# Kernel tuning notes

Hardware: AMD Instinct MI355X
Metric: run time of the kernel (lower is better)

Reference implementation:

```python
import jax, jax.numpy as jnp
import numpy as np

N_HEAD = 16
R = 4  # reciprocal rank

def setup_inputs() -> dict:
    key = jax.random.key(0)
    ks = jax.random.split(key, 8)
    B, T, C = 2, 2048, 1024
    H = N_HEAD
    D = C // H
    D_std = D - R
    x = jax.random.normal(ks[0], (B, T, C), dtype=jnp.float32)
    W_attn = jax.random.normal(ks[1], (3 * C, C), dtype=jnp.float32) * (1.0 / np.sqrt(C))
    W_proj = jax.random.normal(ks[2], (C, C), dtype=jnp.float32) * (1.0 / np.sqrt(C))
    w_std = jnp.full((H,), D_std / D, dtype=jnp.float32)
    w_rec = jnp.full((H,), R / D, dtype=jnp.float32)
    skip_std = jnp.float32(2.0)
    skip_low = jnp.float32(-3.0)
    rwr_alpha = jnp.full((H,), 0.05, dtype=jnp.float32)
    return {"x": x, "W_attn": W_attn, "W_proj": W_proj, "w_std": w_std,
            "w_rec": w_rec, "skip_std": skip_std, "skip_low": skip_low,
            "rwr_alpha": rwr_alpha}

def reference(x, W_attn, W_proj, w_std, w_rec, skip_std, skip_low, rwr_alpha):
    B, T, C = x.shape
    H = N_HEAD
    D = C // H
    D_std = D - R
    # fused QKV projection: [Qf | Kf | V]
    fused = jnp.einsum('btc,fc->btf', x, W_attn)
    qf, kf, v = jnp.split(fused, 3, axis=-1)
    Qf = qf.reshape(B, T, H, D).transpose(0, 2, 1, 3)  # (B,H,T,D)
    Kf = kf.reshape(B, T, H, D).transpose(0, 2, 1, 3)
    V = v.reshape(B, T, H, D).transpose(0, 2, 1, 3)
    # dynamic per-head gate scaling folded into Qf/Kf
    g_std = jnp.sqrt(jnp.clip(w_std * jax.nn.sigmoid(skip_std), 1e-8))  # (H,)
    g_rec = jnp.sqrt(jnp.clip(w_rec * jax.nn.sigmoid(skip_low), 1e-8))  # (H,)
    scale = jnp.concatenate([
        jnp.broadcast_to(g_std[:, None], (H, D_std)),
        jnp.broadcast_to(g_rec[:, None], (H, R)),
    ], axis=-1)  # (H, D)
    scale = scale[None, :, None, :]  # (1,H,1,D)
    Qf = Qf * scale
    Kf = Kf * scale
    # causal SDPA (scale = 1/sqrt(head_dim), dropout=0)
    scores = jnp.einsum('bhqd,bhkd->bhqk', Qf, Kf) / jnp.sqrt(jnp.float32(D))
    causal = jnp.tril(jnp.ones((T, T), dtype=bool))
    scores = jnp.where(causal[None, None], scores, jnp.float32(-1e30))
    attn = jax.nn.softmax(scores, axis=-1)
    y = jnp.einsum('bhqk,bhkd->bhqd', attn, V)
    # self-restart mix: out = (1-alpha)*attn_out + alpha*V, alpha in [0, 0.5]
    alpha = jnp.clip(rwr_alpha, 0.0, 0.5)[None, :, None, None]
    y = (1.0 - alpha) * y + alpha * V
    y = y.transpose(0, 2, 1, 3).reshape(B, T, C)
    return jnp.einsum('btc,oc->bto', y, W_proj)
```

## Files before the change

kernel.cpp:

```cpp
#include <hip/hip_runtime.h>
#include <hip/hip_bf16.h>
#include <math.h>
#include <stdint.h>

#define B_    2
#define T_    2048
#define C_    1024
#define H_    16
#define D_    64
#define R_    4
#define DSTD  60
#define F_    3072
#define BT_   (B_ * T_)

#define LOG2E 1.44269504088896340736f

typedef __bf16 bf16x8 __attribute__((ext_vector_type(8)));
typedef __bf16 bf16x4 __attribute__((ext_vector_type(4)));
typedef float  f32x4  __attribute__((ext_vector_type(4)));

__device__ __forceinline__ int swz(int row, int blk) {
    return blk ^ ((row >> 1) & 7);
}

__device__ __forceinline__ void st_pair(__bf16* p, __bf16 a, __bf16 b) {
    union { __bf16 h[2]; uint32_t u; } t;
    t.h[0] = a; t.h[1] = b;
    *(uint32_t*)p = t.u;
}

__device__ __forceinline__ void gload_lds16(const void* g, void* l) {
    __builtin_amdgcn_global_load_lds(
        (const __attribute__((address_space(1))) uint32_t*)g,
        (__attribute__((address_space(3))) uint32_t*)l, 16, 0, 0);
}

__global__ __launch_bounds__(256) void cast3_kernel(
    const float* __restrict__ a, int na4,
    const float* __restrict__ b, int nb4,
    const float* __restrict__ c, int nc4,
    __bf16* __restrict__ oa, __bf16* __restrict__ ob, __bf16* __restrict__ oc)
{
    int i = blockIdx.x * 256 + threadIdx.x;
    const float* s; __bf16* d; int j = i;
    if (j < na4) { s = a; d = oa; }
    else {
        j -= na4;
        if (j < nb4) { s = b; d = ob; }
        else {
            j -= nb4;
            if (j >= nc4) return;
            s = c; d = oc;
        }
    }
    float4 v = ((const float4*)s)[j];
    bf16x4 o;
    o[0] = (__bf16)v.x; o[1] = (__bf16)v.y;
    o[2] = (__bf16)v.z; o[3] = (__bf16)v.w;
    ((bf16x4*)d)[j] = o;
}

__global__ __launch_bounds__(256) void gemm_qkv_kernel(
    const __bf16* __restrict__ A,
    const __bf16* __restrict__ Bw,
    const float* __restrict__ w_std, const float* __restrict__ w_rec,
    const float* __restrict__ skip_std, const float* __restrict__ skip_low,
    __bf16* __restrict__ Q, __bf16* __restrict__ K, __bf16* __restrict__ V)
{
    __shared__ __bf16 As[128 * 32];
    __shared__ __bf16 Bs[128 * 32];

    const int tid  = threadIdx.x;
    const int row0 = blockIdx.x * 128;
    const int col0 = blockIdx.y * 128;

    const int w    = tid >> 6;
    const int lane = tid & 63;
    const int quad = lane >> 4;
    const int lt   = lane & 15;
    const int wm   = w >> 1;
    const int wn   = w & 1;

    const int lrow = tid >> 2;
    const int lcol = (tid & 3) * 8;

    f32x4 acc[4][4];
#pragma unroll
    for (int i = 0; i < 4; ++i)
#pragma unroll
        for (int j = 0; j < 4; ++j)
#pragma unroll
            for (int r = 0; r < 4; ++r) acc[i][j][r] = 0.f;

    for (int kt = 0; kt < C_ / 32; ++kt) {
        const int k0 = kt * 32;
        __syncthreads();
#pragma unroll
        for (int rr = 0; rr < 2; ++rr) {
            gload_lds16(A  + (size_t)(row0 + rr * 64 + lrow) * C_ + k0 + lcol,
                        As + rr * 2048 + tid * 8);
            gload_lds16(Bw + (size_t)(col0 + rr * 64 + lrow) * C_ + k0 + lcol,
                        Bs + rr * 2048 + tid * 8);
        }
        __syncthreads();

        bf16x8 af[4], bf[4];
#pragma unroll
        for (int i = 0; i < 4; ++i)
            af[i] = *(const bf16x8*)&As[(wm * 64 + i * 16 + lt) * 32 + quad * 8];
#pragma unroll
        for (int j = 0; j < 4; ++j)
            bf[j] = *(const bf16x8*)&Bs[(wn * 64 + j * 16 + lt) * 32 + quad * 8];
#pragma unroll
        for (int i = 0; i < 4; ++i)
#pragma unroll
            for (int j = 0; j < 4; ++j)
                acc[i][j] = __builtin_amdgcn_mfma_f32_16x16x32_bf16(af[i], bf[j], acc[i][j], 0, 0, 0);
    }

    const int colbase = col0 + wn * 64;
    const int which   = colbase >> 10;
    const int h       = (colbase & (C_ - 1)) >> 6;

    const float ss = 1.f / (1.f + __expf(-skip_std[0]));
    const float sl = 1.f / (1.f + __expf(-skip_low[0]));
    const float gs = sqrtf(fmaxf(w_std[h] * ss, 1e-8f));
    const float gr = sqrtf(fmaxf(w_rec[h] * sl, 1e-8f));

    __bf16* dstM = (which == 0) ? Q : (which == 1) ? K : V;

#pragma unroll
    for (int i = 0; i < 4; ++i) {
#pragma unroll
        for (int r = 0; r < 4; ++r) {
            const int row = row0 + wm * 64 + i * 16 + quad * 4 + r;
            const int b = row >> 11;
            const int t = row & (T_ - 1);
            __bf16* dp = dstM + (((size_t)b * H_ + h) * T_ + t) * D_;
#pragma unroll
            for (int j = 0; j < 4; ++j) {
                const int d = j * 16 + lt;
                float val = acc[i][j][r];
                if (which == 0)      val *= ((d < DSTD) ? gs : gr) * (0.125f * LOG2E);
                else if (which == 1) val *= (d < DSTD) ? gs : gr;
                dp[d] = (__bf16)val;
            }
        }
    }
}

__global__ __launch_bounds__(256) void gemm_out_kernel(
    const __bf16* __restrict__ A,
    const __bf16* __restrict__ Bw,
    float* __restrict__ out)
{
    __shared__ __bf16 As[128 * 32];
    __shared__ __bf16 Bs[128 * 32];

    const int tid  = threadIdx.x;
    const int row0 = blockIdx.x * 128;
    const int col0 = blockIdx.y * 128;

    const int w    = tid >> 6;
    const int lane = tid & 63;
    const int quad = lane >> 4;
    const int lt   = lane & 15;
    const int wm   = w >> 1;
    const int wn   = w & 1;

    const int lrow = tid >> 2;
    const int lcol = (tid & 3) * 8;

    f32x4 acc[4][4];
#pragma unroll
    for (int i = 0; i < 4; ++i)
#pragma unroll
        for (int j = 0; j < 4; ++j)
#pragma unroll
            for (int r = 0; r < 4; ++r) acc[i][j][r] = 0.f;

    for (int kt = 0; kt < C_ / 32; ++kt) {
        const int k0 = kt * 32;
        __syncthreads();
#pragma unroll
        for (int rr = 0; rr < 2; ++rr) {
            gload_lds16(A  + (size_t)(row0 + rr * 64 + lrow) * C_ + k0 + lcol,
                        As + rr * 2048 + tid * 8);
            gload_lds16(Bw + (size_t)(col0 + rr * 64 + lrow) * C_ + k0 + lcol,
                        Bs + rr * 2048 + tid * 8);
        }
        __syncthreads();

        bf16x8 af[4], bf[4];
#pragma unroll
        for (int i = 0; i < 4; ++i)
            af[i] = *(const bf16x8*)&As[(wm * 64 + i * 16 + lt) * 32 + quad * 8];
#pragma unroll
        for (int j = 0; j < 4; ++j)
            bf[j] = *(const bf16x8*)&Bs[(wn * 64 + j * 16 + lt) * 32 + quad * 8];
#pragma unroll
        for (int i = 0; i < 4; ++i)
#pragma unroll
            for (int j = 0; j < 4; ++j)
                acc[i][j] = __builtin_amdgcn_mfma_f32_16x16x32_bf16(af[i], bf[j], acc[i][j], 0, 0, 0);
    }

#pragma unroll
    for (int i = 0; i < 4; ++i)
#pragma unroll
        for (int r = 0; r < 4; ++r) {
            const int row = row0 + wm * 64 + i * 16 + quad * 4 + r;
            float* op = out + (size_t)row * C_ + col0 + wn * 64 + lt;
#pragma unroll
            for (int j = 0; j < 4; ++j)
                op[j * 16] = acc[i][j][r];
        }
}

__global__ __launch_bounds__(256) void attn_kernel(
    const __bf16* __restrict__ Q, const __bf16* __restrict__ K,
    const __bf16* __restrict__ V, const float* __restrict__ rwr_alpha,
    __bf16* __restrict__ Y)
{
    __shared__ __align__(16) __bf16 Ks[2][64][64];
    __shared__ __align__(16) __bf16 Vt[2][64][64];
    __shared__ __align__(16) __bf16 Ps[4][16][64];

    const int tid = threadIdx.x;
    const int bh  = blockIdx.x & 31;
    const int g   = blockIdx.x >> 5;
    const int qt  = (g < 8) ? (31 - g) : (g < 16) ? (g - 8)
                  : (g < 24) ? (39 - g) : (g - 16);
    const int h   = bh & (H_ - 1);
    const int b   = bh >> 4;

    const __bf16* Qb = Q + (((size_t)b * H_ + h) * T_) * D_;
    const __bf16* Kb = K + (((size_t)b * H_ + h) * T_) * D_;
    const __bf16* Vb = V + (((size_t)b * H_ + h) * T_) * D_;

    const int w    = tid >> 6;
    const int lane = tid & 63;
    const int quad = lane >> 4;
    const int lt   = lane & 15;

    const int kr0 = tid >> 3;
    const int kc0 = (tid & 7) ^ ((kr0 >> 1) & 7);
    const int kr1 = 32 + kr0;
    const int kc1 = (tid & 7) ^ ((kr1 >> 1) & 7);

    const int kp = (tid >> 3) * 2;
    const int dc = (tid & 7) * 8;
    const int kblk = kp >> 3, koff = kp & 7;

    const __bf16* qrow = Qb + (size_t)(qt * 64 + w * 16 + lt) * D_;
    bf16x8 qf[2];
    qf[0] = *(const bf16x8*)(qrow + quad * 8);
    qf[1] = *(const bf16x8*)(qrow + 32 + quad * 8);

    bf16x8 ones;
#pragma unroll
    for (int u = 0; u < 8; ++u) ones[u] = (__bf16)1.0f;

    gload_lds16(Kb + (size_t)kr0 * 64 + kc0 * 8, &Ks[0][0][0] + tid * 8);
    gload_lds16(Kb + (size_t)kr1 * 64 + kc1 * 8, &Ks[0][32][0] + tid * 8);
    {
        const __bf16* vs = Vb + (size_t)kp * 64 + dc;
        bf16x8 v1 = *(const bf16x8*)(vs);
        bf16x8 v2 = *(const bf16x8*)(vs + 64);
#pragma unroll
        for (int u = 0; u < 8; ++u) {
            const int row = dc + u;
            st_pair(&Vt[0][row][swz(row, kblk) * 8 + koff], v1[u], v2[u]);
        }
    }
    __syncthreads();

    f32x4 lacc;
    f32x4 oacc[4];
#pragma unroll
    for (int r = 0; r < 4; ++r) lacc[r] = 0.f;
#pragma unroll
    for (int n = 0; n < 4; ++n)
#pragma unroll
        for (int r = 0; r < 4; ++r) oacc[n][r] = 0.f;

    for (int kt = 0; kt <= qt; ++kt) {
        const int cur = kt & 1;
        const int nxt = 1 - cur;
        const bool pre = (kt < qt);

        bf16x8 v1, v2;
        if (pre) {
            const size_t toff = (size_t)(kt + 1) * 4096;
            gload_lds16(Kb + toff + (size_t)kr0 * 64 + kc0 * 8, &Ks[nxt][0][0] + tid * 8);
            gload_lds16(Kb + toff + (size_t)kr1 * 64 + kc1 * 8, &Ks[nxt][32][0] + tid * 8);
            const __bf16* vs = Vb + toff + (size_t)kp * 64 + dc;
            v1 = *(const bf16x8*)(vs);
            v2 = *(const bf16x8*)(vs + 64);
        }

        f32x4 sacc[4];
#pragma unroll
        for (int n = 0; n < 4; ++n)
#pragma unroll
            for (int r = 0; r < 4; ++r) sacc[n][r] = 0.f;
#pragma unroll
        for (int kk = 0; kk < 2; ++kk) {
#pragma unroll
            for (int n = 0; n < 4; ++n) {
                const int row = n * 16 + lt;
                bf16x8 ak = *(const bf16x8*)&Ks[cur][row][swz(row, kk * 4 + quad) * 8];
                sacc[n] = __builtin_amdgcn_mfma_f32_16x16x32_bf16(ak, qf[kk], sacc[n], 0, 0, 0);
            }
        }

        if (kt == qt) {
            const int ql = w * 16 + lt;
#pragma unroll
            for (int n = 0; n < 4; ++n) {
                const int keyb = n * 16 + quad * 4;
#pragma unroll
                for (int r = 0; r < 4; ++r)
                    if (keyb + r > ql) sacc[n][r] = -1e30f;
            }
        }

#pragma unroll
        for (int n = 0; n < 4; ++n) {
            bf16x4 pv;
#pragma unroll
            for (int r = 0; r < 4; ++r) pv[r] = (__bf16)exp2f(sacc[n][r]);
            *(bf16x4*)&Ps[w][lt][swz(lt, n * 2 + (quad >> 1)) * 8 + (quad & 1) * 4] = pv;
        }

#pragma unroll
        for (int kk = 0; kk < 2; ++kk) {
            bf16x8 ap = *(const bf16x8*)&Ps[w][lt][swz(lt, kk * 4 + quad) * 8];
            lacc = __builtin_amdgcn_mfma_f32_16x16x32_bf16(ap, ones, lacc, 0, 0, 0);
#pragma unroll
            for (int nd = 0; nd < 4; ++nd) {
                const int drow = nd * 16 + lt;
                bf16x8 bv = *(const bf16x8*)&Vt[cur][drow][swz(drow, kk * 4 + quad) * 8];
                oacc[nd] = __builtin_amdgcn_mfma_f32_16x16x32_bf16(ap, bv, oacc[nd], 0, 0, 0);
            }
        }

        {
            const float lm = fmaxf(fmaxf(lacc[0], lacc[1]), fmaxf(lacc[2], lacc[3]));
            if (__ballot(lm > 1.0e12f)) {
                const float sc = 1.0f / 4294967296.0f;
#pragma unroll
                for (int r = 0; r < 4; ++r) lacc[r] *= sc;
#pragma unroll
                for (int n = 0; n < 4; ++n)
#pragma unroll
                    for (int r = 0; r < 4; ++r) oacc[n][r] *= sc;
            }
        }

        if (pre) {
#pragma unroll
            for (int u = 0; u < 8; ++u) {
                const int row = dc + u;
                st_pair(&Vt[nxt][row][swz(row, kblk) * 8 + koff], v1[u], v2[u]);
            }
        }
        __syncthreads();
    }

    const float a = fminf(fmaxf(rwr_alpha[h], 0.f), 0.5f);
#pragma unroll
    for (int r = 0; r < 4; ++r) {
        const float inv = 1.f / lacc[r];
        const int qg = qt * 64 + w * 16 + quad * 4 + r;
        const __bf16* vp = Vb + (size_t)qg * D_;
        __bf16* yp = Y + ((size_t)(b * T_ + qg)) * C_ + h * D_;
#pragma unroll
        for (int nd = 0; nd < 4; ++nd) {
            const int d = nd * 16 + lt;
            yp[d] = (__bf16)((1.f - a) * oacc[nd][r] * inv + a * (float)vp[d]);
        }
    }
}

extern "C" void kernel_launch(void* const* d_in, const int* in_sizes, int n_in,
                              void* d_out, int out_size, void* d_ws, size_t ws_size,
                              hipStream_t stream) {
    const float* x        = (const float*)d_in[0];
    const float* W_attn   = (const float*)d_in[1];
    const float* W_proj   = (const float*)d_in[2];
    const float* w_std    = (const float*)d_in[3];
    const float* w_rec    = (const float*)d_in[4];
    const float* skip_std = (const float*)d_in[5];
    const float* skip_low = (const float*)d_in[6];
    const float* rwr      = (const float*)d_in[7];
    float* out = (float*)d_out;

    const size_t nX  = (size_t)BT_ * C_;
    const size_t nWa = (size_t)F_ * C_;
    const size_t nWp = (size_t)C_ * C_;
    const size_t per = (size_t)B_ * H_ * T_ * D_;

    __bf16* xb  = (__bf16*)d_ws;
    __bf16* Wab = xb  + nX;
    __bf16* Wpb = Wab + nWa;
    __bf16* Qb  = Wpb + nWp;
    __bf16* Kb  = Qb  + per;
    __bf16* Vb  = Kb  + per;
    __bf16* Yb  = Vb  + per;

    const int na4 = nX / 4, nb4 = nWa / 4, nc4 = nWp / 4;
    cast3_kernel<<<dim3((na4 + nb4 + nc4 + 255) / 256), 256, 0, stream>>>(
        x, na4, W_attn, nb4, W_proj, nc4, xb, Wab, Wpb);

    gemm_qkv_kernel<<<dim3(BT_ / 128, F_ / 128), 256, 0, stream>>>(
        xb, Wab, w_std, w_rec, skip_std, skip_low, Qb, Kb, Vb);
    attn_kernel<<<dim3(32 * (T_ / 64)), 256, 0, stream>>>(Qb, Kb, Vb, rwr, Yb);
    gemm_out_kernel<<<dim3(BT_ / 128, C_ / 128), 256, 0, stream>>>(Yb, Wpb, out);
}
```

Measured before the change: 187.5 us.

## Use 32x32 MFMA in attention with register-resident P via permlane swap

The attention kernel moves from 16x16x32 to 32x32x16 bf16 MFMA, with 2 waves of 32 query rows each instead of 4 waves of 16. The score accumulator is exponentiated, packed to bf16 and rearranged with v_permlane32_swap so it feeds the P·V MFMA directly from registers. This removes the shared-memory P buffer and its store/load round trip. K/V tile loading is redistributed over 128 threads with 4-wide V transposes. The cost is fewer waves per block and higher register pressure from the 16-element accumulators.

```diff
diff --git a/kernel.cpp b/kernel.cpp
--- a/kernel.cpp
+++ b/kernel.cpp
@@ -18,21 +18,26 @@
 typedef __bf16 bf16x8 __attribute__((ext_vector_type(8)));
 typedef __bf16 bf16x4 __attribute__((ext_vector_type(4)));
 typedef float  f32x4  __attribute__((ext_vector_type(4)));
+typedef float  f32x16 __attribute__((ext_vector_type(16)));
 
 __device__ __forceinline__ int swz(int row, int blk) {
     return blk ^ ((row >> 1) & 7);
-}
-
-__device__ __forceinline__ void st_pair(__bf16* p, __bf16 a, __bf16 b) {
-    union { __bf16 h[2]; uint32_t u; } t;
-    t.h[0] = a; t.h[1] = b;
-    *(uint32_t*)p = t.u;
 }
 
 __device__ __forceinline__ void gload_lds16(const void* g, void* l) {
     __builtin_amdgcn_global_load_lds(
         (const __attribute__((address_space(1))) uint32_t*)g,
         (__attribute__((address_space(3))) uint32_t*)l, 16, 0, 0);
+}
+
+__device__ __forceinline__ uint32_t pack2(float lo, float hi) {
+    union { __bf16 h[2]; uint32_t u; } t;
+    t.h[0] = (__bf16)lo; t.h[1] = (__bf16)hi;
+    return t.u;
+}
+
+__device__ __forceinline__ void plswap(uint32_t& a, uint32_t& b) {
+    asm volatile("v_permlane32_swap_b32 %0, %1" : "+v"(a), "+v"(b));
 }
 
 __global__ __launch_bounds__(256) void cast3_kernel(
@@ -217,14 +222,13 @@
         }
 }
 
-__global__ __launch_bounds__(256) void attn_kernel(
+__global__ __launch_bounds__(128) void attn_kernel(
     const __bf16* __restrict__ Q, const __bf16* __restrict__ K,
     const __bf16* __restrict__ V, const float* __restrict__ rwr_alpha,
     __bf16* __restrict__ Y)
 {
     __shared__ __align__(16) __bf16 Ks[2][64][64];
     __shared__ __align__(16) __bf16 Vt[2][64][64];
-    __shared__ __align__(16) __bf16 Ps[4][16][64];
 
     const int tid = threadIdx.x;
     const int bh  = blockIdx.x & 31;
@@ -240,121 +244,139 @@
 
     const int w    = tid >> 6;
     const int lane = tid & 63;
-    const int quad = lane >> 4;
-    const int lt   = lane & 15;
-
-    const int kr0 = tid >> 3;
-    const int kc0 = (tid & 7) ^ ((kr0 >> 1) & 7);
-    const int kr1 = 32 + kr0;
-    const int kc1 = (tid & 7) ^ ((kr1 >> 1) & 7);
-
-    const int kp = (tid >> 3) * 2;
+    const int lq   = lane & 31;
+    const int hi   = lane >> 5;
+
+    const int krb = tid >> 3;
+    const int kcb = tid & 7;
+
+    const int kp = (tid >> 3) * 4;
     const int dc = (tid & 7) * 8;
-    const int kblk = kp >> 3, koff = kp & 7;
-
-    const __bf16* qrow = Qb + (size_t)(qt * 64 + w * 16 + lt) * D_;
-    bf16x8 qf[2];
-    qf[0] = *(const bf16x8*)(qrow + quad * 8);
-    qf[1] = *(const bf16x8*)(qrow + 32 + quad * 8);
+    const int vblk = kp >> 3, voff = kp & 7;
+
+    const __bf16* qrow = Qb + (size_t)(qt * 64 + w * 32 + lq) * D_;
+    bf16x8 qf[4];
+#pragma unroll
+    for (int kk = 0; kk < 4; ++kk)
+        qf[kk] = *(const bf16x8*)(qrow + kk * 16 + hi * 8);
 
     bf16x8 ones;
 #pragma unroll
     for (int u = 0; u < 8; ++u) ones[u] = (__bf16)1.0f;
 
-    gload_lds16(Kb + (size_t)kr0 * 64 + kc0 * 8, &Ks[0][0][0] + tid * 8);
-    gload_lds16(Kb + (size_t)kr1 * 64 + kc1 * 8, &Ks[0][32][0] + tid * 8);
+#pragma unroll
+    for (int cc = 0; cc < 4; ++cc) {
+        const int kr = cc * 16 + krb;
+        const int kc = kcb ^ ((kr >> 1) & 7);
+        gload_lds16(Kb + (size_t)kr * 64 + kc * 8,
+                    &Ks[0][0][0] + cc * 1024 + tid * 8);
+    }
     {
         const __bf16* vs = Vb + (size_t)kp * 64 + dc;
-        bf16x8 v1 = *(const bf16x8*)(vs);
-        bf16x8 v2 = *(const bf16x8*)(vs + 64);
+        bf16x8 v0 = *(const bf16x8*)(vs);
+        bf16x8 v1 = *(const bf16x8*)(vs + 64);
+        bf16x8 v2 = *(const bf16x8*)(vs + 128);
+        bf16x8 v3 = *(const bf16x8*)(vs + 192);
 #pragma unroll
         for (int u = 0; u < 8; ++u) {
             const int row = dc + u;
-            st_pair(&Vt[0][row][swz(row, kblk) * 8 + koff], v1[u], v2[u]);
+            bf16x4 t; t[0] = v0[u]; t[1] = v1[u]; t[2] = v2[u]; t[3] = v3[u];
+            *(bf16x4*)&Vt[0][row][swz(row, vblk) * 8 + voff] = t;
         }
     }
     __syncthreads();
 
-    f32x4 lacc;
-    f32x4 oacc[4];
-#pragma unroll
-    for (int r = 0; r < 4; ++r) lacc[r] = 0.f;
-#pragma unroll
-    for (int n = 0; n < 4; ++n)
-#pragma unroll
-        for (int r = 0; r < 4; ++r) oacc[n][r] = 0.f;
+    f32x16 oacc[2], lacc;
+#pragma unroll
+    for (int r = 0; r < 16; ++r) { oacc[0][r] = 0.f; oacc[1][r] = 0.f; lacc[r] = 0.f; }
 
     for (int kt = 0; kt <= qt; ++kt) {
         const int cur = kt & 1;
-        const int nxt = 1 - cur;
+        const int nxt = cur ^ 1;
         const bool pre = (kt < qt);
 
-        bf16x8 v1, v2;
+        bf16x8 v0, v1, v2, v3;
         if (pre) {
             const size_t toff = (size_t)(kt + 1) * 4096;
-            gload_lds16(Kb + toff + (size_t)kr0 * 64 + kc0 * 8, &Ks[nxt][0][0] + tid * 8);
-            gload_lds16(Kb + toff + (size_t)kr1 * 64 + kc1 * 8, &Ks[nxt][32][0] + tid * 8);
+#pragma unroll
+            for (int cc = 0; cc < 4; ++cc) {
+                const int kr = cc * 16 + krb;
+                const int kc = kcb ^ ((kr >> 1) & 7);
+                gload_lds16(Kb + toff + (size_t)kr * 64 + kc * 8,
+                            &Ks[nxt][0][0] + cc * 1024 + tid * 8);
+            }
             const __bf16* vs = Vb + toff + (size_t)kp * 64 + dc;
-            v1 = *(const bf16x8*)(vs);
-            v2 = *(const bf16x8*)(vs + 64);
-        }
-
-        f32x4 sacc[4];
-#pragma unroll
-        for (int n = 0; n < 4; ++n)
-#pragma unroll
-            for (int r = 0; r < 4; ++r) sacc[n][r] = 0.f;
-#pragma unroll
-        for (int kk = 0; kk < 2; ++kk) {
-#pragma unroll
-            for (int n = 0; n < 4; ++n) {
-                const int row = n * 16 + lt;
-                bf16x8 ak = *(const bf16x8*)&Ks[cur][row][swz(row, kk * 4 + quad) * 8];
-                sacc[n] = __builtin_amdgcn_mfma_f32_16x16x32_bf16(ak, qf[kk], sacc[n], 0, 0, 0);
-            }
-        }
-
-        if (kt == qt) {
-            const int ql = w * 16 + lt;
-#pragma unroll
-            for (int n = 0; n < 4; ++n) {
-                const int keyb = n * 16 + quad * 4;
-#pragma unroll
-                for (int r = 0; r < 4; ++r)
-                    if (keyb + r > ql) sacc[n][r] = -1e30f;
-            }
-        }
-
-#pragma unroll
-        for (int n = 0; n < 4; ++n) {
-            bf16x4 pv;
-#pragma unroll
-            for (int r = 0; r < 4; ++r) pv[r] = (__bf16)exp2f(sacc[n][r]);
-            *(bf16x4*)&Ps[w][lt][swz(lt, n * 2 + (quad >> 1)) * 8 + (quad & 1) * 4] = pv;
-        }
-
-#pragma unroll
-        for (int kk = 0; kk < 2; ++kk) {
-            bf16x8 ap = *(const bf16x8*)&Ps[w][lt][swz(lt, kk * 4 + quad) * 8];
-            lacc = __builtin_amdgcn_mfma_f32_16x16x32_bf16(ap, ones, lacc, 0, 0, 0);
-#pragma unroll
-            for (int nd = 0; nd < 4; ++nd) {
-                const int drow = nd * 16 + lt;
-                bf16x8 bv = *(const bf16x8*)&Vt[cur][drow][swz(drow, kk * 4 + quad) * 8];
-                oacc[nd] = __builtin_amdgcn_mfma_f32_16x16x32_bf16(ap, bv, oacc[nd], 0, 0, 0);
+            v0 = *(const bf16x8*)(vs);
+            v1 = *(const bf16x8*)(vs + 64);
+            v2 = *(const bf16x8*)(vs + 128);
+            v3 = *(const bf16x8*)(vs + 192);
+        }
+
+#pragma unroll
+        for (int kb = 0; kb < 2; ++kb) {
+            f32x16 sacc;
+#pragma unroll
+            for (int r = 0; r < 16; ++r) sacc[r] = 0.f;
+            const int arow = kb * 32 + lq;
+#pragma unroll
+            for (int kk = 0; kk < 4; ++kk) {
+                bf16x8 ak = *(const bf16x8*)&Ks[cur][arow][swz(arow, kk * 2 + hi) * 8];
+                sacc = __builtin_amdgcn_mfma_f32_32x32x16_bf16(ak, qf[kk], sacc, 0, 0, 0);
+            }
+
+            if (kt == qt) {
+                const int ql = w * 32 + lq;
+#pragma unroll
+                for (int r = 0; r < 16; ++r) {
+                    const int key = kb * 32 + (r & 3) + ((r >> 2) << 3) + hi * 4;
+                    if (key > ql) sacc[r] = -1e30f;
+                }
+            }
+
+#pragma unroll
+            for (int c = 0; c < 2; ++c) {
+                const int rb = 8 * c;
+                float p0 = __builtin_amdgcn_exp2f(sacc[rb + 0]);
+                float p1 = __builtin_amdgcn_exp2f(sacc[rb + 1]);
+                float p2 = __builtin_amdgcn_exp2f(sacc[rb + 2]);
+                float p3 = __builtin_amdgcn_exp2f(sacc[rb + 3]);
+                float p4 = __builtin_amdgcn_exp2f(sacc[rb + 4]);
+                float p5 = __builtin_amdgcn_exp2f(sacc[rb + 5]);
+                float p6 = __builtin_amdgcn_exp2f(sacc[rb + 6]);
+                float p7 = __builtin_amdgcn_exp2f(sacc[rb + 7]);
+
+                uint32_t w0 = pack2(p0, p1);
+                uint32_t w2 = pack2(p4, p5);
+                plswap(w0, w2);
+                uint32_t w1 = pack2(p2, p3);
+                uint32_t w3 = pack2(p6, p7);
+                plswap(w1, w3);
+
+                union { uint32_t u[4]; bf16x8 v; } pf;
+                pf.u[0] = w0; pf.u[1] = w1; pf.u[2] = w2; pf.u[3] = w3;
+
+                lacc = __builtin_amdgcn_mfma_f32_32x32x16_bf16(pf.v, ones, lacc, 0, 0, 0);
+
+                const int kk2 = kb * 2 + c;
+#pragma unroll
+                for (int db = 0; db < 2; ++db) {
+                    const int drow = db * 32 + lq;
+                    bf16x8 bv = *(const bf16x8*)&Vt[cur][drow][swz(drow, kk2 * 2 + hi) * 8];
+                    oacc[db] = __builtin_amdgcn_mfma_f32_32x32x16_bf16(pf.v, bv, oacc[db], 0, 0, 0);
+                }
             }
         }
 
         {
-            const float lm = fmaxf(fmaxf(lacc[0], lacc[1]), fmaxf(lacc[2], lacc[3]));
+            float lm = lacc[0];
+#pragma unroll
+            for (int r = 1; r < 16; ++r) lm = fmaxf(lm, lacc[r]);
             if (__ballot(lm > 1.0e12f)) {
                 const float sc = 1.0f / 4294967296.0f;
 #pragma unroll
-                for (int r = 0; r < 4; ++r) lacc[r] *= sc;
-#pragma unroll
-                for (int n = 0; n < 4; ++n)
-#pragma unroll
-                    for (int r = 0; r < 4; ++r) oacc[n][r] *= sc;
+                for (int r = 0; r < 16; ++r) {
+                    lacc[r] *= sc; oacc[0][r] *= sc; oacc[1][r] *= sc;
+                }
             }
         }
 
@@ -362,7 +384,8 @@
 #pragma unroll
             for (int u = 0; u < 8; ++u) {
                 const int row = dc + u;
-                st_pair(&Vt[nxt][row][swz(row, kblk) * 8 + koff], v1[u], v2[u]);
+                bf16x4 t; t[0] = v0[u]; t[1] = v1[u]; t[2] = v2[u]; t[3] = v3[u];
+                *(bf16x4*)&Vt[nxt][row][swz(row, vblk) * 8 + voff] = t;
             }
         }
         __syncthreads();
@@ -370,15 +393,15 @@
 
     const float a = fminf(fmaxf(rwr_alpha[h], 0.f), 0.5f);
 #pragma unroll
-    for (int r = 0; r < 4; ++r) {
+    for (int r = 0; r < 16; ++r) {
         const float inv = 1.f / lacc[r];
-        const int qg = qt * 64 + w * 16 + quad * 4 + r;
+        const int qg = qt * 64 + w * 32 + (r & 3) + ((r >> 2) << 3) + hi * 4;
         const __bf16* vp = Vb + (size_t)qg * D_;
         __bf16* yp = Y + ((size_t)(b * T_ + qg)) * C_ + h * D_;
 #pragma unroll
-        for (int nd = 0; nd < 4; ++nd) {
-            const int d = nd * 16 + lt;
-            yp[d] = (__bf16)((1.f - a) * oacc[nd][r] * inv + a * (float)vp[d]);
+        for (int db = 0; db < 2; ++db) {
+            const int d = db * 32 + lq;
+            yp[d] = (__bf16)((1.f - a) * oacc[db][r] * inv + a * (float)vp[d]);
         }
     }
 }
@@ -415,6 +438,6 @@
 
     gemm_qkv_kernel<<<dim3(BT_ / 128, F_ / 128), 256, 0, stream>>>(
         xb, Wab, w_std, w_rec, skip_std, skip_low, Qb, Kb, Vb);
-    attn_kernel<<<dim3(32 * (T_ / 64)), 256, 0, stream>>>(Qb, Kb, Vb, rwr, Yb);
+    attn_kernel<<<dim3(32 * (T_ / 64)), 128, 0, stream>>>(Qb, Kb, Vb, rwr, Yb);
     gemm_out_kernel<<<dim3(BT_ / 128, C_ / 128), 256, 0, stream>>>(Yb, Wpb, out);
 }
```

Result: slower. 196.8 us (+4.9%).
